# Kernel optimization log

Measured on AMD Instinct MI355X. Metric: run time of the kernel, lower is better.

## Reference

```python
import jax, jax.numpy as jnp
import numpy as np

N_NODES = 100000
NNZ = 3200000
D_FEAT = 128


def setup_inputs() -> dict:
    key = jax.random.key(0)
    k1, k2, k3 = jax.random.split(key, 3)
    indices = jax.random.randint(k1, (2, NNZ), 0, N_NODES, dtype=jnp.int64 if jax.config.jax_enable_x64 else jnp.int32)
    values = jax.random.normal(k2, (NNZ,), dtype=jnp.float32)
    b = jax.random.normal(k3, (N_NODES, D_FEAT), dtype=jnp.float32)
    return {"indices": indices, "values": values, "n_rows": N_NODES, "b": b}


def reference(indices, values, n_rows, b):
    # out = sparse_coo(indices, values, [n_rows, n_rows]) @ b
    # out[i] = sum_{e: row[e]==i} values[e] * b[col[e]]
    row, col = indices[0], indices[1]
    gathered = values[:, None] * b[col]              # [nnz, d]
    out = jax.ops.segment_sum(gathered, row, num_segments=n_rows)  # [n_rows, d]
    return out
```

## Files before the change

### kernel.cpp

```cpp
#include <hip/hip_runtime.h>


#define D_FEAT 128
#define RPB 64
#define BKT_SHIFT 6
#define MAX_NB 2048
#define NBLK_SCAT 512
#define CHUNK_MAX 6400
#define STG_CAP 3072
#define RP_FLAG (1 << 30)

__device__ __forceinline__ unsigned short f2bf(float f) {
    unsigned u = __float_as_uint(f);
    u += 0x7FFFu + ((u >> 16) & 1u);
    return (unsigned short)(u >> 16);
}
__global__ void bconv_kernel(const float* __restrict__ bmat,
                             ushort* __restrict__ b16, int n4) {
    int i = blockIdx.x * blockDim.x + threadIdx.x;
    int gs = gridDim.x * blockDim.x;
    for (int k = i; k < n4; k += gs) {
        float4 v = reinterpret_cast<const float4*>(bmat)[k];
        ushort4 o;
        o.x = f2bf(v.x); o.y = f2bf(v.y); o.z = f2bf(v.z); o.w = f2bf(v.w);
        reinterpret_cast<ushort4*>(b16)[k] = o;
    }
}

__global__ void hist_kernel(const int* __restrict__ rowidx, int* __restrict__ hist,
                            int nnz) {
    __shared__ int lcnt[MAX_NB];
    for (int i = threadIdx.x; i < MAX_NB; i += blockDim.x) lcnt[i] = 0;
    __syncthreads();
    int gid = blockIdx.x * blockDim.x + threadIdx.x;
    int gsz = gridDim.x * blockDim.x;
    for (int e = gid; e < nnz; e += gsz)
        atomicAdd(&lcnt[rowidx[e] >> BKT_SHIFT], 1);
    __syncthreads();
    for (int i = threadIdx.x; i < MAX_NB; i += blockDim.x)
        if (lcnt[i]) atomicAdd(&hist[i], lcnt[i]);
}

__global__ void scan_kernel(const int* __restrict__ hist, int* __restrict__ gbase,
                            int* __restrict__ gcursor, int nb) {
    __shared__ int hs[1024];
    int t = threadIdx.x;
    int c0 = hist[2 * t], c1 = hist[2 * t + 1];
    hs[t] = c0 + c1;
    __syncthreads();
    for (int off = 1; off < 1024; off <<= 1) {
        int u = (t >= off) ? hs[t - off] : 0;
        __syncthreads();
        hs[t] += u;
        __syncthreads();
    }
    int excl = hs[t] - (c0 + c1);
    if (2 * t < nb)     { gbase[2 * t] = excl;          gcursor[2 * t] = excl; }
    if (2 * t + 1 < nb) { gbase[2 * t + 1] = excl + c0; gcursor[2 * t + 1] = excl + c0; }
}

__global__ __launch_bounds__(512)
void scatter_kernel(const int* __restrict__ rowidx, const int* __restrict__ colidx,
                    const float* __restrict__ vals, int* __restrict__ gcursor,
                    float2* __restrict__ cv, int nnz, int nb) {
    __shared__ int loff[MAX_NB];
    __shared__ int cur[MAX_NB];
    __shared__ int gpos[MAX_NB];
    __shared__ float2 stage[CHUNK_MAX];
    int* scanbuf = (int*)stage;

    int t = threadIdx.x;
    int chunk = (nnz + gridDim.x - 1) / gridDim.x;
    int beg = blockIdx.x * chunk;
    int end = min(beg + chunk, nnz);

    for (int i = t; i < MAX_NB; i += 512) loff[i] = 0;
    __syncthreads();
    for (int e = beg + t; e < end; e += 512)
        atomicAdd(&loff[rowidx[e] >> BKT_SHIFT], 1);
    __syncthreads();

    int c0 = loff[4 * t], c1 = loff[4 * t + 1], c2 = loff[4 * t + 2], c3 = loff[4 * t + 3];
    int s = c0 + c1 + c2 + c3;
    scanbuf[t] = s;
    __syncthreads();
    for (int off = 1; off < 512; off <<= 1) {
        int u = (t >= off) ? scanbuf[t - off] : 0;
        __syncthreads();
        scanbuf[t] += u;
        __syncthreads();
    }
    int excl = scanbuf[t] - s;
    __syncthreads();
    loff[4 * t] = excl;
    loff[4 * t + 1] = excl + c0;
    loff[4 * t + 2] = excl + c0 + c1;
    loff[4 * t + 3] = excl + c0 + c1 + c2;
    __syncthreads();
    for (int i = t; i < MAX_NB; i += 512) cur[i] = loff[i];
    __syncthreads();

    for (int e = beg + t; e < end; e += 512) {
        int r = rowidx[e];
        int bkt = r >> BKT_SHIFT;
        int pos = atomicAdd(&cur[bkt], 1);
        int pack = ((r & (RPB - 1)) << 17) | colidx[e];
        stage[pos] = make_float2(__int_as_float(pack), vals[e]);
    }
    __syncthreads();

    int w = t >> 6, lane = t & 63;
    int bpw = (nb + 7) >> 3;
    int wbeg = w * bpw, wend = min(wbeg + bpw, nb);
    for (int b0 = wbeg; b0 < wend; b0 += 64) {
        int bkt = b0 + lane;
        if (bkt < wend) {
            int n = cur[bkt] - loff[bkt];
            int g = 0;
            if (n > 0) g = atomicAdd(&gcursor[bkt], n);
            gpos[bkt] = g;
        }
    }
    __syncthreads();
    for (int bkt = wbeg; bkt < wend; ++bkt) {
        int sOff = loff[bkt], n = cur[bkt] - sOff;
        if (n <= 0) continue;
        int g = gpos[bkt];
        for (int k = lane; k < n; k += 64) cv[g + k] = stage[sOff + k];
    }
}

__global__ __launch_bounds__(256)
void rowsort_kernel(const int* __restrict__ gbase, const int* __restrict__ gend,
                    float2* __restrict__ cv, int* __restrict__ rowptr,
                    int n_rows, int nb) {
    __shared__ float2 stg[STG_CAP];
    __shared__ int cnt[RPB];
    __shared__ int base[RPB];
    __shared__ int cur[RPB];
    int t = threadIdx.x;
    int bkt = blockIdx.x;
    int beg = gbase[bkt], end = gend[bkt];
    int n = end - beg;

    if (bkt == nb - 1 && t == 0) rowptr[n_rows] = end;

    if (n > STG_CAP) {
        if (t < RPB) {
            int row = bkt * RPB + t;
            if (row < n_rows) rowptr[row] = beg | RP_FLAG;
        }
        return;
    }

    if (t < RPB) cnt[t] = 0;
    __syncthreads();
    for (int i = t; i < n; i += 256) {
        float2 p = cv[beg + i];
        stg[i] = p;
        atomicAdd(&cnt[__float_as_int(p.x) >> 17], 1);
    }
    __syncthreads();
    if (t == 0) {
        int run = 0;
        for (int i = 0; i < RPB; ++i) { base[i] = run; cur[i] = run; run += cnt[i]; }
    }
    __syncthreads();
    if (t < RPB) {
        int row = bkt * RPB + t;
        if (row < n_rows) rowptr[row] = beg + base[t];
    }
    for (int i = t; i < n; i += 256) {
        float2 p = stg[i];
        int pos = atomicAdd(&cur[__float_as_int(p.x) >> 17], 1);
        cv[beg + pos] = p;
    }
}

__device__ __forceinline__ float bf2f(unsigned short h) {
    return __uint_as_float((unsigned)h << 16);
}
__global__ __launch_bounds__(256)
void rowmm16_kernel(const int* __restrict__ rowptr, const int* __restrict__ gbase,
                    const int* __restrict__ gend, const float2* __restrict__ cv,
                    const ushort* __restrict__ b16, float* __restrict__ out,
                    int n_rows) {
    int wid  = (blockIdx.x * blockDim.x + threadIdx.x) >> 6;
    int lane = threadIdx.x & 63;
    if (wid >= n_rows) return;

    const ushort2* bp = reinterpret_cast<const ushort2*>(b16) + lane;
    float2 acc = make_float2(0.f, 0.f);

    int rp = rowptr[wid];
    if (rp & RP_FLAG) {
        int bkt = wid >> BKT_SHIFT;
        int beg = gbase[bkt], end = gend[bkt];
        int myrl = wid & (RPB - 1);
        for (int j = beg; j < end; ++j) {
            float2 p = cv[j];
            int pack = __float_as_int(p.x);
            if ((pack >> 17) == myrl) {
                ushort2 u = bp[(size_t)(pack & 0x1FFFF) * (D_FEAT / 2)];
                acc.x += p.y * bf2f(u.x);  acc.y += p.y * bf2f(u.y);
            }
        }
    } else {
        int beg = rp;
        int end = rowptr[wid + 1] & ~RP_FLAG;
        int j = beg;
        for (; j + 7 < end; j += 8) {
            float2 p0 = cv[j],     p1 = cv[j + 1];
            float2 p2 = cv[j + 2], p3 = cv[j + 3];
            float2 p4 = cv[j + 4], p5 = cv[j + 5];
            float2 p6 = cv[j + 6], p7 = cv[j + 7];
            ushort2 u0 = bp[(size_t)(__float_as_int(p0.x) & 0x1FFFF) * (D_FEAT / 2)];
            ushort2 u1 = bp[(size_t)(__float_as_int(p1.x) & 0x1FFFF) * (D_FEAT / 2)];
            ushort2 u2 = bp[(size_t)(__float_as_int(p2.x) & 0x1FFFF) * (D_FEAT / 2)];
            ushort2 u3 = bp[(size_t)(__float_as_int(p3.x) & 0x1FFFF) * (D_FEAT / 2)];
            ushort2 u4 = bp[(size_t)(__float_as_int(p4.x) & 0x1FFFF) * (D_FEAT / 2)];
            ushort2 u5 = bp[(size_t)(__float_as_int(p5.x) & 0x1FFFF) * (D_FEAT / 2)];
            ushort2 u6 = bp[(size_t)(__float_as_int(p6.x) & 0x1FFFF) * (D_FEAT / 2)];
            ushort2 u7 = bp[(size_t)(__float_as_int(p7.x) & 0x1FFFF) * (D_FEAT / 2)];
            acc.x += p0.y * bf2f(u0.x);  acc.y += p0.y * bf2f(u0.y);
            acc.x += p1.y * bf2f(u1.x);  acc.y += p1.y * bf2f(u1.y);
            acc.x += p2.y * bf2f(u2.x);  acc.y += p2.y * bf2f(u2.y);
            acc.x += p3.y * bf2f(u3.x);  acc.y += p3.y * bf2f(u3.y);
            acc.x += p4.y * bf2f(u4.x);  acc.y += p4.y * bf2f(u4.y);
            acc.x += p5.y * bf2f(u5.x);  acc.y += p5.y * bf2f(u5.y);
            acc.x += p6.y * bf2f(u6.x);  acc.y += p6.y * bf2f(u6.y);
            acc.x += p7.y * bf2f(u7.x);  acc.y += p7.y * bf2f(u7.y);
        }
        for (; j < end; ++j) {
            float2 p = cv[j];
            ushort2 u = bp[(size_t)(__float_as_int(p.x) & 0x1FFFF) * (D_FEAT / 2)];
            acc.x += p.y * bf2f(u.x);  acc.y += p.y * bf2f(u.y);
        }
    }
    reinterpret_cast<float2*>(out + (size_t)wid * D_FEAT)[lane] = acc;
}

__global__ __launch_bounds__(256)
void rowmm_kernel(const int* __restrict__ rowptr, const int* __restrict__ gbase,
                  const int* __restrict__ gend, const float2* __restrict__ cv,
                  const float* __restrict__ bmat, float* __restrict__ out,
                  int n_rows) {
    int wid  = (blockIdx.x * blockDim.x + threadIdx.x) >> 6;
    int lane = threadIdx.x & 63;
    if (wid >= n_rows) return;
    const float2* bp = reinterpret_cast<const float2*>(bmat) + lane;
    float2 acc = make_float2(0.f, 0.f);
    int rp = rowptr[wid];
    if (rp & RP_FLAG) {
        int bkt = wid >> BKT_SHIFT;
        int beg = gbase[bkt], end = gend[bkt];
        int myrl = wid & (RPB - 1);
        for (int j = beg; j < end; ++j) {
            float2 p = cv[j];
            int pack = __float_as_int(p.x);
            if ((pack >> 17) == myrl) {
                float2 v = bp[(size_t)(pack & 0x1FFFF) * (D_FEAT / 2)];
                acc.x += p.y * v.x;  acc.y += p.y * v.y;
            }
        }
    } else {
        int beg = rp, end = rowptr[wid + 1] & ~RP_FLAG;
        for (int j = beg; j < end; ++j) {
            float2 p = cv[j];
            float2 v = bp[(size_t)(__float_as_int(p.x) & 0x1FFFF) * (D_FEAT / 2)];
            acc.x += p.y * v.x;  acc.y += p.y * v.y;
        }
    }
    reinterpret_cast<float2*>(out + (size_t)wid * D_FEAT)[lane] = acc;
}

extern "C" void kernel_launch(void* const* d_in, const int* in_sizes, int n_in,
                              void* d_out, int out_size, void* d_ws, size_t ws_size,
                              hipStream_t stream) {
    const int*   indices = (const int*)d_in[0];
    const float* values  = (const float*)d_in[1];
    const float* b       = (const float*)d_in[3];
    float*       out     = (float*)d_out;

    const int nnz    = in_sizes[1];
    const int n_rows = out_size / D_FEAT;
    const int nb     = (n_rows + RPB - 1) / RPB;
    const int* rowidx = indices;
    const int* colidx = indices + nnz;

    int*    hist    = (int*)d_ws;
    int*    gbase   = hist + MAX_NB;
    int*    gcursor = gbase + MAX_NB;
    int*    rowptr  = gcursor + MAX_NB;
    size_t  off     = (3 * MAX_NB + (size_t)n_rows + 1) * sizeof(int);
    off = (off + 15) & ~(size_t)15;

    size_t b16_bytes = (size_t)n_rows * D_FEAT * sizeof(ushort);
    size_t cv_bytes  = (size_t)nnz * sizeof(float2);
    bool   use16     = (off + b16_bytes + cv_bytes) <= ws_size;

    ushort* b16 = (ushort*)((char*)d_ws + off);
    float2* cv  = (float2*)((char*)d_ws + off + (use16 ? b16_bytes : 0));

    hipMemsetAsync(hist, 0, MAX_NB * sizeof(int), stream);
    if (use16)
        bconv_kernel<<<2048, 256, 0, stream>>>(b, b16, n_rows * D_FEAT / 4);
    hist_kernel<<<512, 256, 0, stream>>>(rowidx, hist, nnz);
    scan_kernel<<<1, 1024, 0, stream>>>(hist, gbase, gcursor, nb);
    scatter_kernel<<<NBLK_SCAT, 512, 0, stream>>>(rowidx, colidx, values, gcursor, cv, nnz, nb);
    rowsort_kernel<<<nb, 256, 0, stream>>>(gbase, gcursor, cv, rowptr, n_rows, nb);
    if (use16)
        rowmm16_kernel<<<(n_rows * 64 + 255) / 256, 256, 0, stream>>>(rowptr, gbase, gcursor,
                                                                      cv, b16, out, n_rows);
    else
        rowmm_kernel<<<(n_rows * 64 + 255) / 256, 256, 0, stream>>>(rowptr, gbase, gcursor,
                                                                    cv, b, out, n_rows);
}
```

Measured before the change: 285.7 us.

## Widen row buckets to 256 rows and flatten scatter write-out with per-element bucket tags

```diff
diff --git a/kernel.cpp b/kernel.cpp
--- a/kernel.cpp
+++ b/kernel.cpp
@@ -2,12 +2,12 @@
 
 
 #define D_FEAT 128
-#define RPB 64
-#define BKT_SHIFT 6
-#define MAX_NB 2048
+#define RPB 256
+#define BKT_SHIFT 8
+#define MAX_NB 512
 #define NBLK_SCAT 512
 #define CHUNK_MAX 6400
-#define STG_CAP 3072
+#define STG_CAP 12288
 #define RP_FLAG (1 << 30)
 
 __device__ __forceinline__ unsigned short f2bf(float f) {
@@ -43,20 +43,19 @@
 
 __global__ void scan_kernel(const int* __restrict__ hist, int* __restrict__ gbase,
                             int* __restrict__ gcursor, int nb) {
-    __shared__ int hs[1024];
+    __shared__ int hs[512];
     int t = threadIdx.x;
-    int c0 = hist[2 * t], c1 = hist[2 * t + 1];
-    hs[t] = c0 + c1;
-    __syncthreads();
-    for (int off = 1; off < 1024; off <<= 1) {
+    int v = hist[t];
+    hs[t] = v;
+    __syncthreads();
+    for (int off = 1; off < 512; off <<= 1) {
         int u = (t >= off) ? hs[t - off] : 0;
         __syncthreads();
         hs[t] += u;
         __syncthreads();
     }
-    int excl = hs[t] - (c0 + c1);
-    if (2 * t < nb)     { gbase[2 * t] = excl;          gcursor[2 * t] = excl; }
-    if (2 * t + 1 < nb) { gbase[2 * t + 1] = excl + c0; gcursor[2 * t + 1] = excl + c0; }
+    int excl = hs[t] - v;
+    if (t < nb) { gbase[t] = excl; gcursor[t] = excl; }
 }
 
 __global__ __launch_bounds__(512)
@@ -66,6 +65,7 @@
     __shared__ int loff[MAX_NB];
     __shared__ int cur[MAX_NB];
     __shared__ int gpos[MAX_NB];
+    __shared__ ushort bktof[CHUNK_MAX];
     __shared__ float2 stage[CHUNK_MAX];
     int* scanbuf = (int*)stage;
 
@@ -73,6 +73,7 @@
     int chunk = (nnz + gridDim.x - 1) / gridDim.x;
     int beg = blockIdx.x * chunk;
     int end = min(beg + chunk, nnz);
+    int n = end - beg;
 
     for (int i = t; i < MAX_NB; i += 512) loff[i] = 0;
     __syncthreads();
@@ -80,9 +81,8 @@
         atomicAdd(&loff[rowidx[e] >> BKT_SHIFT], 1);
     __syncthreads();
 
-    int c0 = loff[4 * t], c1 = loff[4 * t + 1], c2 = loff[4 * t + 2], c3 = loff[4 * t + 3];
-    int s = c0 + c1 + c2 + c3;
-    scanbuf[t] = s;
+    int v = loff[t];
+    scanbuf[t] = v;
     __syncthreads();
     for (int off = 1; off < 512; off <<= 1) {
         int u = (t >= off) ? scanbuf[t - off] : 0;
@@ -90,14 +90,10 @@
         scanbuf[t] += u;
         __syncthreads();
     }
-    int excl = scanbuf[t] - s;
-    __syncthreads();
-    loff[4 * t] = excl;
-    loff[4 * t + 1] = excl + c0;
-    loff[4 * t + 2] = excl + c0 + c1;
-    loff[4 * t + 3] = excl + c0 + c1 + c2;
-    __syncthreads();
-    for (int i = t; i < MAX_NB; i += 512) cur[i] = loff[i];
+    int excl = scanbuf[t] - v;
+    __syncthreads();
+    loff[t] = excl;
+    cur[t] = excl;
     __syncthreads();
 
     for (int e = beg + t; e < end; e += 512) {
@@ -106,27 +102,19 @@
         int pos = atomicAdd(&cur[bkt], 1);
         int pack = ((r & (RPB - 1)) << 17) | colidx[e];
         stage[pos] = make_float2(__int_as_float(pack), vals[e]);
-    }
-    __syncthreads();
-
-    int w = t >> 6, lane = t & 63;
-    int bpw = (nb + 7) >> 3;
-    int wbeg = w * bpw, wend = min(wbeg + bpw, nb);
-    for (int b0 = wbeg; b0 < wend; b0 += 64) {
-        int bkt = b0 + lane;
-        if (bkt < wend) {
-            int n = cur[bkt] - loff[bkt];
-            int g = 0;
-            if (n > 0) g = atomicAdd(&gcursor[bkt], n);
-            gpos[bkt] = g;
-        }
-    }
-    __syncthreads();
-    for (int bkt = wbeg; bkt < wend; ++bkt) {
-        int sOff = loff[bkt], n = cur[bkt] - sOff;
-        if (n <= 0) continue;
-        int g = gpos[bkt];
-        for (int k = lane; k < n; k += 64) cv[g + k] = stage[sOff + k];
+        bktof[pos] = (ushort)bkt;
+    }
+    __syncthreads();
+
+    if (t < nb) {
+        int cnt = cur[t] - loff[t];
+        if (cnt > 0) gpos[t] = atomicAdd(&gcursor[t], cnt);
+    }
+    __syncthreads();
+
+    for (int i = t; i < n; i += 512) {
+        int bkt = bktof[i];
+        cv[gpos[bkt] + (i - loff[bkt])] = stage[i];
     }
 }
 
@@ -135,8 +123,8 @@
                     float2* __restrict__ cv, int* __restrict__ rowptr,
                     int n_rows, int nb) {
     __shared__ float2 stg[STG_CAP];
-    __shared__ int cnt[RPB];
-    __shared__ int base[RPB];
+    __shared__ int bin[RPB];
+    __shared__ int sc[RPB];
     __shared__ int cur[RPB];
     int t = threadIdx.x;
     int bkt = blockIdx.x;
@@ -146,30 +134,33 @@
     if (bkt == nb - 1 && t == 0) rowptr[n_rows] = end;
 
     if (n > STG_CAP) {
-        if (t < RPB) {
-            int row = bkt * RPB + t;
-            if (row < n_rows) rowptr[row] = beg | RP_FLAG;
-        }
+        int row = bkt * RPB + t;
+        if (row < n_rows) rowptr[row] = beg | RP_FLAG;
         return;
     }
 
-    if (t < RPB) cnt[t] = 0;
+    bin[t] = 0;
     __syncthreads();
     for (int i = t; i < n; i += 256) {
         float2 p = cv[beg + i];
         stg[i] = p;
-        atomicAdd(&cnt[__float_as_int(p.x) >> 17], 1);
-    }
-    __syncthreads();
-    if (t == 0) {
-        int run = 0;
-        for (int i = 0; i < RPB; ++i) { base[i] = run; cur[i] = run; run += cnt[i]; }
-    }
-    __syncthreads();
-    if (t < RPB) {
-        int row = bkt * RPB + t;
-        if (row < n_rows) rowptr[row] = beg + base[t];
-    }
+        atomicAdd(&bin[__float_as_int(p.x) >> 17], 1);
+    }
+    __syncthreads();
+    int v = bin[t];
+    sc[t] = v;
+    __syncthreads();
+    for (int off = 1; off < 256; off <<= 1) {
+        int u = (t >= off) ? sc[t - off] : 0;
+        __syncthreads();
+        sc[t] += u;
+        __syncthreads();
+    }
+    int excl = sc[t] - v;
+    cur[t] = excl;
+    int row = bkt * RPB + t;
+    if (row < n_rows) rowptr[row] = beg + excl;
+    __syncthreads();
     for (int i = t; i < n; i += 256) {
         float2 p = stg[i];
         int pos = atomicAdd(&cur[__float_as_int(p.x) >> 17], 1);
@@ -304,9 +295,9 @@
 
     hipMemsetAsync(hist, 0, MAX_NB * sizeof(int), stream);
     if (use16)
-        bconv_kernel<<<2048, 256, 0, stream>>>(b, b16, n_rows * D_FEAT / 4);
+        bconv_kernel<<<1024, 256, 0, stream>>>(b, b16, n_rows * D_FEAT / 4);
     hist_kernel<<<512, 256, 0, stream>>>(rowidx, hist, nnz);
-    scan_kernel<<<1, 1024, 0, stream>>>(hist, gbase, gcursor, nb);
+    scan_kernel<<<1, 512, 0, stream>>>(hist, gbase, gcursor, nb);
     scatter_kernel<<<NBLK_SCAT, 512, 0, stream>>>(rowidx, colidx, values, gcursor, cv, nnz, nb);
     rowsort_kernel<<<nb, 256, 0, stream>>>(gbase, gcursor, cv, rowptr, n_rows, nb);
     if (use16)
```

After: 255.5 us. 10.6% less time.
